# Performance work log

Hardware: AMD Instinct MI355X
Metric: run time of the kernel (lower is better)

Reference implementation:

```python
import jax, jax.numpy as jnp
import numpy as np

NUM_HEADS = 8


def setup_inputs() -> dict:
    key = jax.random.key(0)
    ks = jax.random.split(key, 6)
    B, C, H, W = 64, 512, 16, 16
    x = jax.random.normal(ks[0], (B, C, H, W), dtype=jnp.float32)
    qkv_w = jax.random.normal(ks[1], (3 * C, C), dtype=jnp.float32) * (C ** -0.5)
    qkv_b = jax.random.normal(ks[2], (3 * C,), dtype=jnp.float32) * 0.02
    out_w = jax.random.normal(ks[3], (C, C), dtype=jnp.float32) * (C ** -0.5)
    out_b = jax.random.normal(ks[4], (C,), dtype=jnp.float32) * 0.02
    rel_pos_enc = jax.random.normal(ks[5], (NUM_HEADS, 2 * 16 - 1, 2 * 16 - 1), dtype=jnp.float32) * 0.02
    return {"x": x, "qkv_w": qkv_w, "qkv_b": qkv_b, "out_w": out_w,
            "out_b": out_b, "rel_pos_enc": rel_pos_enc}


def _attention(x, qkv_w, qkv_b, out_w, out_b, rel_pos_enc):
    B, C, H, W = x.shape
    heads = rel_pos_enc.shape[0]
    hd = C // heads
    N = H * W

    # 1x1 conv qkv projection == pointwise GEMM over channels
    qkv = jnp.einsum('bchw,oc->bohw', x, qkv_w) + qkv_b[None, :, None, None]
    q, k, v = jnp.split(qkv, 3, axis=1)  # each (B, C, H, W)
    q = q.reshape(B, heads, hd, N)
    k = k.reshape(B, heads, hd, N)
    v = v.reshape(B, heads, hd, N)

    attn = jnp.einsum('bhdn,bhdm->bhnm', q, k) * (hd ** -0.5)  # (B,h,N,N)

    # gathered 2D relative position bias: bias[head,(h1,w1),(h2,w2)] =
    #   rel_pos_enc[head, h1-h2+15, w1-w2+15]
    h_idx = (jnp.arange(H)[:, None] - jnp.arange(H)[None, :]) + 16 - 1  # (H,H)
    w_idx = (jnp.arange(W)[:, None] - jnp.arange(W)[None, :]) + 16 - 1  # (W,W)
    bias = rel_pos_enc[:, h_idx[:, None, :, None], w_idx[None, :, None, :]]  # (h,H,W,H,W)
    bias = bias.reshape(heads, N, N)

    attn = jax.nn.softmax(attn + bias[None], axis=-1)
    out = jnp.einsum('bhnm,bhdm->bhdn', attn, v).reshape(B, C, H, W)
    out = jnp.einsum('bchw,oc->bohw', out, out_w) + out_b[None, :, None, None]
    return out


def reference(x, qkv_w, qkv_b, out_w, out_b, rel_pos_enc):
    return _attention(x, qkv_w, qkv_b, out_w, out_b, rel_pos_enc)
```

## Files before the change

### kernel.cpp

```cpp
#include <hip/hip_runtime.h>

typedef __attribute__((ext_vector_type(8))) short short8;
typedef __attribute__((ext_vector_type(4))) float floatx4;
typedef __attribute__((ext_vector_type(4))) int   intx4;

#define MFMA16(a,b,c) __builtin_amdgcn_mfma_f32_16x16x32_bf16((a),(b),(c),0,0,0)

static __device__ __forceinline__ unsigned short f2bf(float f){
    unsigned int u = __float_as_uint(f);
    u = (u + 0x7FFFu + ((u >> 16) & 1u)) >> 16;
    return (unsigned short)u;
}

static __device__ __forceinline__ unsigned int pkbf(float lo, float hi){
    unsigned int r;
    asm("v_cvt_pk_bf16_f32 %0, %1, %2" : "=v"(r) : "v"(lo), "v"(hi));
    return r;
}

static __device__ __forceinline__ void async16(const unsigned short* g, const unsigned short* l){
    __builtin_amdgcn_global_load_lds(
        (const __attribute__((address_space(1))) unsigned int*)g,
        (__attribute__((address_space(3))) unsigned int*)l, 16, 0, 0);
}

__global__ __launch_bounds__(256) void k_prep(const float* __restrict__ x,
                                              unsigned short* __restrict__ xT,
                                              const float* __restrict__ qkvw,
                                              unsigned short* __restrict__ wqkv,
                                              const float* __restrict__ outw,
                                              unsigned short* __restrict__ wout){
    __shared__ unsigned short tile[64][78];
    const int bid = blockIdx.x;
    const int tid = threadIdx.x;
    if (bid < 2048){
        const int c0 = (bid & 7) * 64;
        const int n0 = ((bid >> 3) & 3) * 64;
        const int b  = bid >> 5;
        const int chunk = tid & 7;
        const int r     = tid >> 3;
        const float*    src = x  + (size_t)b * 131072;
        unsigned short* dst = xT + (size_t)b * 131072;
#pragma unroll
        for (int it = 0; it < 2; ++it){
            int c = r + it * 32;
            const float* p = src + (size_t)(c0 + c) * 256 + n0 + chunk * 8;
            float4 f0 = *(const float4*)(p);
            float4 f1 = *(const float4*)(p + 4);
            short8 v;
            v[0]=(short)f2bf(f0.x); v[1]=(short)f2bf(f0.y); v[2]=(short)f2bf(f0.z); v[3]=(short)f2bf(f0.w);
            v[4]=(short)f2bf(f1.x); v[5]=(short)f2bf(f1.y); v[6]=(short)f2bf(f1.z); v[7]=(short)f2bf(f1.w);
            *(short8*)&tile[c][chunk * 8] = v;
        }
        __syncthreads();
#pragma unroll
        for (int it = 0; it < 2; ++it){
            int n = r + it * 32;
            short8 o;
#pragma unroll
            for (int e = 0; e < 8; ++e) o[e] = (short)tile[chunk * 8 + e][n];
            *(short8*)(dst + (size_t)(n0 + n) * 512 + c0 + chunk * 8) = o;
        }
    } else {
        int i = (bid - 2048) * 256 + tid;
        const float* s; unsigned short* d; int j;
        if (i < 196608){ s = qkvw; d = wqkv; j = i; }
        else { j = i - 196608; if (j >= 65536) return; s = outw; d = wout; }
        float4 f = *(const float4*)(s + (size_t)j * 4);
        uint2 v;
        v.x = (unsigned int)f2bf(f.x) | ((unsigned int)f2bf(f.y) << 16);
        v.y = (unsigned int)f2bf(f.z) | ((unsigned int)f2bf(f.w) << 16);
        *(uint2*)(d + (size_t)j * 4) = v;
    }
}

__global__ __launch_bounds__(512, 2) void k_fused(const unsigned short* __restrict__ xT,
                                                  const unsigned short* __restrict__ wbf,
                                                  const float* __restrict__ qkvb,
                                                  const float* __restrict__ rel,
                                                  unsigned short* __restrict__ ao){
    __shared__ unsigned short SH[79748];
    const int XS = 0;
    const int WS = 16384;
    const int QS = 28672;
    const int KS = 45056;
    const int VS = 61440;
    float* Relsh = (float*)&SH[77824];

    const int bid  = blockIdx.x;
    const int xcd  = bid & 7;
    const int slot = bid >> 3;
    const int b = xcd * 8 + (slot & 7);
    const int h = slot >> 3;
    const int tid  = threadIdx.x;
    const int wave = tid >> 6;
    const int lane = tid & 63;
    const int lrow = lane & 15;
    const int lgrp = lane >> 4;
    const int mq = wave >> 1;
    const int nh = wave & 1;

    for (int i = tid; i < 961; i += 512) Relsh[i] = rel[h * 961 + i] * 1.44269504f;

    floatx4 acc[4][6];
#pragma unroll
    for (int i = 0; i < 4; ++i)
#pragma unroll
        for (int j = 0; j < 6; ++j){ floatx4 z = {0.f,0.f,0.f,0.f}; acc[i][j] = z; }

    const unsigned short* xb = xT + (size_t)(b * 256) * 512;
    const unsigned short* xsrc[4]; int xdo[4];
#pragma unroll
    for (int c = 0; c < 4; ++c){
        int s   = (c * 8 + wave) * 64 + lane;
        int row = s >> 3, pch = s & 7;
        int sch = pch ^ (row & 7);
        xsrc[c] = xb + (size_t)row * 512 + sch * 8;
        xdo[c]  = (c * 8 + wave) * 512;
    }
    const unsigned short* wsrc[3]; int wdo[3];
#pragma unroll
    for (int c = 0; c < 3; ++c){
        int s   = (c * 8 + wave) * 64 + lane;
        int row = s >> 3, pch = s & 7;
        int sch = pch ^ (row & 7);
        int grow = (row >> 6) * 512 + h * 64 + (row & 63);
        wsrc[c] = wbf + (size_t)grow * 512 + sch * 8;
        wdo[c]  = (c * 8 + wave) * 512;
    }

    auto stageA = [&](int XBs, int WBs, int kk){
#pragma unroll
        for (int c = 0; c < 4; ++c) async16(xsrc[c] + kk, &SH[XBs + xdo[c]]);
#pragma unroll
        for (int c = 0; c < 3; ++c) async16(wsrc[c] + kk, &SH[WBs + wdo[c]]);
    };
    auto compA = [&](int XBs, int WBs){
#pragma unroll
        for (int ks = 0; ks < 2; ++ks){
            short8 af[4], bq[6];
#pragma unroll
            for (int mt = 0; mt < 4; ++mt){
                int row = mq * 64 + mt * 16 + lrow;
                int pch = (ks * 4 + lgrp) ^ (row & 7);
                af[mt] = *(const short8*)&SH[XBs + row * 64 + pch * 8];
            }
#pragma unroll
            for (int nt = 0; nt < 6; ++nt){
                int row = nh * 96 + nt * 16 + lrow;
                int pch = (ks * 4 + lgrp) ^ (row & 7);
                bq[nt] = *(const short8*)&SH[WBs + row * 64 + pch * 8];
            }
#pragma unroll
            for (int mt = 0; mt < 4; ++mt)
#pragma unroll
                for (int nt = 0; nt < 6; ++nt)
                    acc[mt][nt] = MFMA16(af[mt], bq[nt], acc[mt][nt]);
        }
    };

    stageA(XS, WS, 0);
    __syncthreads();
#pragma unroll
    for (int t2 = 0; t2 < 4; ++t2){
        stageA(QS, KS, t2 * 128 + 64);
        compA(XS, WS);
        __syncthreads();
        if (t2 < 3) stageA(XS, WS, t2 * 128 + 128);
        compA(QS, KS);
        __syncthreads();
    }

#pragma unroll
    for (int mt = 0; mt < 4; ++mt){
#pragma unroll
        for (int nt = 0; nt < 6; ++nt){
            int col = nh * 96 + nt * 16 + lrow;
            int seg = col >> 6, off = col & 63;
            float bv = qkvb[seg * 512 + h * 64 + off];
            int token0 = mq * 64 + mt * 16 + lgrp * 4;
            if (seg == 2){
                int lch = token0 >> 3;
                int pch = (lch & 24) | ((lch & 7) ^ (off & 7));
                uint2 vv;
                vv.x = pkbf(acc[mt][nt][0] + bv, acc[mt][nt][1] + bv);
                vv.y = pkbf(acc[mt][nt][2] + bv, acc[mt][nt][3] + bv);
                *(uint2*)&SH[VS + off * 256 + pch * 8 + (lgrp & 1) * 4] = vv;
            } else if (seg == 1){
#pragma unroll
                for (int r = 0; r < 4; ++r){
                    int token = token0 + r;
                    int kslot = (token & ~0x1C) | ((token & 4) << 2) | ((token & 0x18) >> 1);
                    int pch   = (off >> 3) ^ (kslot & 7);
                    SH[KS + kslot * 64 + pch * 8 + (off & 7)] = f2bf(acc[mt][nt][r] + bv);
                }
            } else {
#pragma unroll
                for (int r = 0; r < 4; ++r){
                    int token = token0 + r;
                    int pch   = (off >> 3) ^ (token & 7);
                    SH[QS + token * 64 + pch * 8 + (off & 7)] =
                        f2bf((acc[mt][nt][r] + bv) * 0.18033688f);
                }
            }
        }
    }
    __syncthreads();

    short8 aq[2][2];
#pragma unroll
    for (int pp = 0; pp < 2; ++pp)
#pragma unroll
        for (int kc = 0; kc < 2; ++kc){
            int row = wave * 32 + pp * 16 + lrow;
            int pch = (kc * 4 + lgrp) ^ (row & 7);
            aq[pp][kc] = *(const short8*)&SH[QS + row * 64 + pch * 8];
        }

    unsigned short* aob = ao + (size_t)(b * 256) * 512 + h * 64;
    const int khB = lgrp >> 1;
    const int kwB = (lgrp & 1) * 8;

#pragma unroll
    for (int pp = 0; pp < 2; ++pp){
        floatx4 st[16];
        __builtin_amdgcn_s_setprio(1);
#pragma unroll
        for (int ct = 0; ct < 16; ++ct){
            int row  = ct * 16 + lrow;
            int pch0 = lgrp ^ (row & 7);
            short8 k0 = *(const short8*)&SH[KS + row * 64 + pch0 * 8];
            short8 k1 = *(const short8*)&SH[KS + row * 64 + (pch0 ^ 4) * 8];
            floatx4 z = {0.f,0.f,0.f,0.f};
            z = MFMA16(k0, aq[pp][0], z);
            z = MFMA16(k1, aq[pp][1], z);
            st[ct] = z;
        }
        __builtin_amdgcn_s_setprio(0);

        float sum = 0.f;
        const int rbase = (wave * 2 + pp + 15) * 31 + lrow + 15 - kwB;
#pragma unroll
        for (int ct = 0; ct < 16; ++ct){
            int rb = rbase - (2 * (ct >> 1) + khB) * 31 - 4 * (ct & 1);
#pragma unroll
            for (int r = 0; r < 4; ++r){
                float e = __builtin_amdgcn_exp2f(st[ct][r] + Relsh[rb - r]);
                st[ct][r] = e;
                sum += e;
            }
        }
        sum += __shfl_xor(sum, 16, 64);
        sum += __shfl_xor(sum, 32, 64);
        float inv = 1.f / sum;

        intx4 pf[8];
#pragma unroll
        for (int ms = 0; ms < 8; ++ms){
            intx4 t;
            t.x = (int)pkbf(st[2*ms  ][0], st[2*ms  ][1]);
            t.y = (int)pkbf(st[2*ms  ][2], st[2*ms  ][3]);
            t.z = (int)pkbf(st[2*ms+1][0], st[2*ms+1][1]);
            t.w = (int)pkbf(st[2*ms+1][2], st[2*ms+1][3]);
            pf[ms] = t;
        }

        const int n = wave * 32 + pp * 16 + lrow;
        __builtin_amdgcn_s_setprio(1);
#pragma unroll
        for (int dt = 0; dt < 4; ++dt){
            floatx4 accO = {0.f,0.f,0.f,0.f};
#pragma unroll
            for (int ms = 0; ms < 8; ++ms){
                int row = dt * 16 + lrow;
                int lch = ms * 4 + lgrp;
                int pch = (lch & 24) | ((lch & 7) ^ (row & 7));
                short8 vb = *(const short8*)&SH[VS + row * 256 + pch * 8];
                accO = MFMA16(vb, __builtin_bit_cast(short8, pf[ms]), accO);
            }
            uint2 ov;
            ov.x = pkbf(accO[0] * inv, accO[1] * inv);
            ov.y = pkbf(accO[2] * inv, accO[3] * inv);
            *(uint2*)(aob + (size_t)n * 512 + dt * 16 + lgrp * 4) = ov;
        }
        __builtin_amdgcn_s_setprio(0);
    }
}

__global__ __launch_bounds__(256, 2) void k_out(const unsigned short* __restrict__ ao,
                                                const unsigned short* __restrict__ wbf,
                                                const float* __restrict__ bias,
                                                float* __restrict__ out){
    __shared__ unsigned short Ash[2][2][128][32];
    __shared__ unsigned short Bsh[2][2][128][32];
    const int bid  = blockIdx.x;
    const int xcd  = bid & 7;
    const int slot = bid >> 3;
    const int t0 = (xcd * 16 + (slot & 15)) * 128;
    const int o0 = (slot >> 4) * 128;
    const int tid  = threadIdx.x;
    const int wave = tid >> 6;
    const int lane = tid & 63;
    const int lrow = lane & 15;
    const int wm   = (wave >> 1) * 64;
    const int wn   = (wave & 1) * 64;
    const int ld_row = wave * 32 + (lane >> 2);
    const int ld_col = (((lane & 3) ^ ((lane >> 3) & 3))) * 8;
    const int pcho = (((lane >> 4) ^ ((lrow >> 1) & 3))) * 8;

    floatx4 acc[4][4];
#pragma unroll
    for (int i = 0; i < 4; ++i)
#pragma unroll
        for (int j = 0; j < 4; ++j){ floatx4 z = {0.f,0.f,0.f,0.f}; acc[i][j] = z; }

    const unsigned short* gA = wbf + (size_t)(o0 + ld_row) * 512 + ld_col;
    const unsigned short* gB = ao  + (size_t)(t0 + ld_row) * 512 + ld_col;

    auto stage = [&](int d, int kk){
        async16(gA + kk,                 &Ash[d][0][wave * 32][0]);
        async16(gA + kk + 16 * 512,      &Ash[d][0][wave * 32 + 16][0]);
        async16(gA + kk + 32,            &Ash[d][1][wave * 32][0]);
        async16(gA + kk + 32 + 16 * 512, &Ash[d][1][wave * 32 + 16][0]);
        async16(gB + kk,                 &Bsh[d][0][wave * 32][0]);
        async16(gB + kk + 16 * 512,      &Bsh[d][0][wave * 32 + 16][0]);
        async16(gB + kk + 32,            &Bsh[d][1][wave * 32][0]);
        async16(gB + kk + 32 + 16 * 512, &Bsh[d][1][wave * 32 + 16][0]);
    };
    auto comp = [&](int d){
#pragma unroll
        for (int s = 0; s < 2; ++s){
            short8 af[4], bq[4];
#pragma unroll
            for (int mt = 0; mt < 4; ++mt) af[mt] = *(const short8*)&Ash[d][s][wm + mt*16 + lrow][pcho];
#pragma unroll
            for (int nt = 0; nt < 4; ++nt) bq[nt] = *(const short8*)&Bsh[d][s][wn + nt*16 + lrow][pcho];
#pragma unroll
            for (int mt = 0; mt < 4; ++mt)
#pragma unroll
                for (int nt = 0; nt < 4; ++nt)
                    acc[mt][nt] = MFMA16(af[mt], bq[nt], acc[mt][nt]);
        }
    };

    stage(0, 0);
    __syncthreads();
#pragma unroll
    for (int t2 = 0; t2 < 4; ++t2){
        stage(1, t2 * 128 + 64);
        comp(0);
        __syncthreads();
        if (t2 < 3) stage(0, t2 * 128 + 128);
        comp(1);
        __syncthreads();
    }
#pragma unroll
    for (int mt = 0; mt < 4; ++mt){
        int orow0 = o0 + wm + mt*16 + (lane >> 4) * 4;
#pragma unroll
        for (int nt = 0; nt < 4; ++nt){
            int tcol = t0 + wn + nt*16 + lrow;
            int bb = tcol >> 8, nn = tcol & 255;
#pragma unroll
            for (int r = 0; r < 4; ++r){
                float bv = bias[orow0 + r];
                out[(size_t)(bb * 512 + orow0 + r) * 256 + nn] = acc[mt][nt][r] + bv;
            }
        }
    }
}

extern "C" void kernel_launch(void* const* d_in, const int* in_sizes, int n_in,
                              void* d_out, int out_size, void* d_ws, size_t ws_size,
                              hipStream_t stream){
    const float* x    = (const float*)d_in[0];
    const float* qkvw = (const float*)d_in[1];
    const float* qkvb = (const float*)d_in[2];
    const float* outw = (const float*)d_in[3];
    const float* outb = (const float*)d_in[4];
    const float* rel  = (const float*)d_in[5];
    float* out = (float*)d_out;

    const size_t XT_OFF = 0;
    const size_t AO_OFF = 16777216;
    const size_t W_OFF  = 33554432;
    const size_t NEED   = W_OFF + 4194304;
    if (ws_size < NEED) return;

    char* ws = (char*)d_ws;
    unsigned short* xT = (unsigned short*)(ws + XT_OFF);
    unsigned short* ao = (unsigned short*)(ws + AO_OFF);
    unsigned short* wqkv_bf = (unsigned short*)(ws + W_OFF);
    unsigned short* wout_bf = (unsigned short*)(ws + W_OFF + 2097152);

    hipLaunchKernelGGL(k_prep,  dim3(3072), dim3(256), 0, stream,
                       x, xT, qkvw, wqkv_bf, outw, wout_bf);
    hipLaunchKernelGGL(k_fused, dim3(512),  dim3(512), 0, stream,
                       xT, wqkv_bf, qkvb, rel, ao);
    hipLaunchKernelGGL(k_out,   dim3(512),  dim3(256), 0, stream,
                       ao, wout_bf, outb, out);
}
```

Baseline: 151.2 us.

## Precompute bias matrix as MFMA init and deepen GEMM load pipelining

The prep kernel now expands the relative-position bias into a bf16 (heads,256,256) table, pre-scaled by log2(e). The fused kernel loads this table from global memory and uses it as the MFMA accumulator init, so the per-element shared-memory bias gather and add in the softmax loop go away. Both query sub-tiles are processed together so each V fragment read feeds two MFMAs. The GEMM stage loops in the fused and output kernels now issue two stages ahead and use explicit vmcnt waits with raw barriers instead of __syncthreads. Costs are more global bias traffic, bf16 rounding of the bias, and higher register pressure.

```diff
diff --git a/kernel.cpp b/kernel.cpp
--- a/kernel.cpp
+++ b/kernel.cpp
@@ -29,7 +29,9 @@
                                               const float* __restrict__ qkvw,
                                               unsigned short* __restrict__ wqkv,
                                               const float* __restrict__ outw,
-                                              unsigned short* __restrict__ wout){
+                                              unsigned short* __restrict__ wout,
+                                              const float* __restrict__ rel,
+                                              unsigned short* __restrict__ Bp){
     __shared__ unsigned short tile[64][78];
     const int bid = blockIdx.x;
     const int tid = threadIdx.x;
@@ -61,7 +63,7 @@
             for (int e = 0; e < 8; ++e) o[e] = (short)tile[chunk * 8 + e][n];
             *(short8*)(dst + (size_t)(n0 + n) * 512 + c0 + chunk * 8) = o;
         }
-    } else {
+    } else if (bid < 3072){
         int i = (bid - 2048) * 256 + tid;
         const float* s; unsigned short* d; int j;
         if (i < 196608){ s = qkvw; d = wqkv; j = i; }
@@ -71,21 +73,34 @@
         v.x = (unsigned int)f2bf(f.x) | ((unsigned int)f2bf(f.y) << 16);
         v.y = (unsigned int)f2bf(f.z) | ((unsigned int)f2bf(f.w) << 16);
         *(uint2*)(d + (size_t)j * 4) = v;
+    } else {
+        int idx   = (bid - 3072) * 256 + tid;
+        int h     = idx >> 14;
+        int token = (idx >> 6) & 255;
+        int key0  = (idx & 63) << 2;
+        int th = token >> 4, tw = token & 15;
+        int kh = key0 >> 4,  kw0 = key0 & 15;
+        int base = h * 961 + (th - kh + 15) * 31 + (tw - kw0 + 15);
+        float v0 = rel[base]     * 1.44269504f;
+        float v1 = rel[base - 1] * 1.44269504f;
+        float v2 = rel[base - 2] * 1.44269504f;
+        float v3 = rel[base - 3] * 1.44269504f;
+        uint2 o; o.x = pkbf(v0, v1); o.y = pkbf(v2, v3);
+        *(uint2*)(Bp + (size_t)idx * 4) = o;
     }
 }
 
 __global__ __launch_bounds__(512, 2) void k_fused(const unsigned short* __restrict__ xT,
                                                   const unsigned short* __restrict__ wbf,
                                                   const float* __restrict__ qkvb,
-                                                  const float* __restrict__ rel,
+                                                  const unsigned short* __restrict__ Bp,
                                                   unsigned short* __restrict__ ao){
-    __shared__ unsigned short SH[79748];
+    __shared__ unsigned short SH[77824];
     const int XS = 0;
     const int WS = 16384;
     const int QS = 28672;
     const int KS = 45056;
     const int VS = 61440;
-    float* Relsh = (float*)&SH[77824];
 
     const int bid  = blockIdx.x;
     const int xcd  = bid & 7;
@@ -100,8 +115,6 @@
     const int mq = wave >> 1;
     const int nh = wave & 1;
 
-    for (int i = tid; i < 961; i += 512) Relsh[i] = rel[h * 961 + i] * 1.44269504f;
-
     floatx4 acc[4][6];
 #pragma unroll
     for (int i = 0; i < 4; ++i)
@@ -160,15 +173,27 @@
     };
 
     stageA(XS, WS, 0);
-    __syncthreads();
+    stageA(QS, KS, 64);
 #pragma unroll
     for (int t2 = 0; t2 < 4; ++t2){
-        stageA(QS, KS, t2 * 128 + 64);
+        asm volatile("s_waitcnt vmcnt(7)" ::: "memory");
+        __builtin_amdgcn_s_barrier();
+        asm volatile("" ::: "memory");
         compA(XS, WS);
-        __syncthreads();
-        if (t2 < 3) stageA(XS, WS, t2 * 128 + 128);
+        asm volatile("" ::: "memory");
+        if (t2 < 3){
+            __builtin_amdgcn_s_barrier();
+            stageA(XS, WS, t2 * 128 + 128);
+            asm volatile("s_waitcnt vmcnt(7)" ::: "memory");
+        } else {
+            asm volatile("s_waitcnt vmcnt(0)" ::: "memory");
+        }
+        __builtin_amdgcn_s_barrier();
+        asm volatile("" ::: "memory");
         compA(QS, KS);
-        __syncthreads();
+        asm volatile("" ::: "memory");
+        __builtin_amdgcn_s_barrier();
+        if (t2 < 3) stageA(QS, KS, t2 * 128 + 192);
     }
 
 #pragma unroll
@@ -217,74 +242,106 @@
             aq[pp][kc] = *(const short8*)&SH[QS + row * 64 + pch * 8];
         }
 
+    const unsigned short* bp0 = Bp + ((size_t)h * 256 + wave * 32 + lrow) * 256;
+
+    floatx4 st0[16], st1[16];
+    __builtin_amdgcn_s_setprio(1);
+#pragma unroll
+    for (int ct = 0; ct < 16; ++ct){
+        int key0 = 32 * (ct >> 1) + 8 * lgrp + 4 * (ct & 1);
+        uint2 bA = *(const uint2*)(bp0 + key0);
+        uint2 bB = *(const uint2*)(bp0 + 4096 + key0);
+        int row  = ct * 16 + lrow;
+        int pch0 = lgrp ^ (row & 7);
+        short8 k0 = *(const short8*)&SH[KS + row * 64 + pch0 * 8];
+        short8 k1 = *(const short8*)&SH[KS + row * 64 + (pch0 ^ 4) * 8];
+        floatx4 z0, z1;
+        z0[0] = __uint_as_float(bA.x << 16);
+        z0[1] = __uint_as_float(bA.x & 0xFFFF0000u);
+        z0[2] = __uint_as_float(bA.y << 16);
+        z0[3] = __uint_as_float(bA.y & 0xFFFF0000u);
+        z1[0] = __uint_as_float(bB.x << 16);
+        z1[1] = __uint_as_float(bB.x & 0xFFFF0000u);
+        z1[2] = __uint_as_float(bB.y << 16);
+        z1[3] = __uint_as_float(bB.y & 0xFFFF0000u);
+        z0 = MFMA16(k0, aq[0][0], z0);
+        z0 = MFMA16(k1, aq[0][1], z0);
+        z1 = MFMA16(k0, aq[1][0], z1);
+        z1 = MFMA16(k1, aq[1][1], z1);
+        st0[ct] = z0; st1[ct] = z1;
+    }
+    __builtin_amdgcn_s_setprio(0);
+
+    float inv0, inv1;
+    {
+        float p0=0.f,p1=0.f,p2=0.f,p3=0.f;
+#pragma unroll
+        for (int ct = 0; ct < 16; ++ct){
+            float e0 = __builtin_amdgcn_exp2f(st0[ct][0]); st0[ct][0]=e0; p0+=e0;
+            float e1 = __builtin_amdgcn_exp2f(st0[ct][1]); st0[ct][1]=e1; p1+=e1;
+            float e2 = __builtin_amdgcn_exp2f(st0[ct][2]); st0[ct][2]=e2; p2+=e2;
+            float e3 = __builtin_amdgcn_exp2f(st0[ct][3]); st0[ct][3]=e3; p3+=e3;
+        }
+        float s = (p0+p1)+(p2+p3);
+        s += __shfl_xor(s, 16, 64);
+        s += __shfl_xor(s, 32, 64);
+        inv0 = 1.f / s;
+    }
+    {
+        float p0=0.f,p1=0.f,p2=0.f,p3=0.f;
+#pragma unroll
+        for (int ct = 0; ct < 16; ++ct){
+            float e0 = __builtin_amdgcn_exp2f(st1[ct][0]); st1[ct][0]=e0; p0+=e0;
+            float e1 = __builtin_amdgcn_exp2f(st1[ct][1]); st1[ct][1]=e1; p1+=e1;
+            float e2 = __builtin_amdgcn_exp2f(st1[ct][2]); st1[ct][2]=e2; p2+=e2;
+            float e3 = __builtin_amdgcn_exp2f(st1[ct][3]); st1[ct][3]=e3; p3+=e3;
+        }
+        float s = (p0+p1)+(p2+p3);
+        s += __shfl_xor(s, 16, 64);
+        s += __shfl_xor(s, 32, 64);
+        inv1 = 1.f / s;
+    }
+
+    intx4 pf0[8], pf1[8];
+#pragma unroll
+    for (int ms = 0; ms < 8; ++ms){
+        intx4 t0_, t1_;
+        t0_.x = (int)pkbf(st0[2*ms  ][0], st0[2*ms  ][1]);
+        t0_.y = (int)pkbf(st0[2*ms  ][2], st0[2*ms  ][3]);
+        t0_.z = (int)pkbf(st0[2*ms+1][0], st0[2*ms+1][1]);
+        t0_.w = (int)pkbf(st0[2*ms+1][2], st0[2*ms+1][3]);
+        pf0[ms] = t0_;
+        t1_.x = (int)pkbf(st1[2*ms  ][0], st1[2*ms  ][1]);
+        t1_.y = (int)pkbf(st1[2*ms  ][2], st1[2*ms  ][3]);
+        t1_.z = (int)pkbf(st1[2*ms+1][0], st1[2*ms+1][1]);
+        t1_.w = (int)pkbf(st1[2*ms+1][2], st1[2*ms+1][3]);
+        pf1[ms] = t1_;
+    }
+
     unsigned short* aob = ao + (size_t)(b * 256) * 512 + h * 64;
-    const int khB = lgrp >> 1;
-    const int kwB = (lgrp & 1) * 8;
-
-#pragma unroll
-    for (int pp = 0; pp < 2; ++pp){
-        floatx4 st[16];
-        __builtin_amdgcn_s_setprio(1);
-#pragma unroll
-        for (int ct = 0; ct < 16; ++ct){
-            int row  = ct * 16 + lrow;
-            int pch0 = lgrp ^ (row & 7);
-            short8 k0 = *(const short8*)&SH[KS + row * 64 + pch0 * 8];
-            short8 k1 = *(const short8*)&SH[KS + row * 64 + (pch0 ^ 4) * 8];
-            floatx4 z = {0.f,0.f,0.f,0.f};
-            z = MFMA16(k0, aq[pp][0], z);
-            z = MFMA16(k1, aq[pp][1], z);
-            st[ct] = z;
-        }
-        __builtin_amdgcn_s_setprio(0);
-
-        float sum = 0.f;
-        const int rbase = (wave * 2 + pp + 15) * 31 + lrow + 15 - kwB;
-#pragma unroll
-        for (int ct = 0; ct < 16; ++ct){
-            int rb = rbase - (2 * (ct >> 1) + khB) * 31 - 4 * (ct & 1);
-#pragma unroll
-            for (int r = 0; r < 4; ++r){
-                float e = __builtin_amdgcn_exp2f(st[ct][r] + Relsh[rb - r]);
-                st[ct][r] = e;
-                sum += e;
-            }
-        }
-        sum += __shfl_xor(sum, 16, 64);
-        sum += __shfl_xor(sum, 32, 64);
-        float inv = 1.f / sum;
-
-        intx4 pf[8];
+    const int n0 = wave * 32 + lrow;
+    __builtin_amdgcn_s_setprio(1);
+#pragma unroll
+    for (int dt = 0; dt < 4; ++dt){
+        floatx4 a0 = {0.f,0.f,0.f,0.f}, a1 = {0.f,0.f,0.f,0.f};
 #pragma unroll
         for (int ms = 0; ms < 8; ++ms){
-            intx4 t;
-            t.x = (int)pkbf(st[2*ms  ][0], st[2*ms  ][1]);
-            t.y = (int)pkbf(st[2*ms  ][2], st[2*ms  ][3]);
-            t.z = (int)pkbf(st[2*ms+1][0], st[2*ms+1][1]);
-            t.w = (int)pkbf(st[2*ms+1][2], st[2*ms+1][3]);
-            pf[ms] = t;
-        }
-
-        const int n = wave * 32 + pp * 16 + lrow;
-        __builtin_amdgcn_s_setprio(1);
-#pragma unroll
-        for (int dt = 0; dt < 4; ++dt){
-            floatx4 accO = {0.f,0.f,0.f,0.f};
-#pragma unroll
-            for (int ms = 0; ms < 8; ++ms){
-                int row = dt * 16 + lrow;
-                int lch = ms * 4 + lgrp;
-                int pch = (lch & 24) | ((lch & 7) ^ (row & 7));
-                short8 vb = *(const short8*)&SH[VS + row * 256 + pch * 8];
-                accO = MFMA16(vb, __builtin_bit_cast(short8, pf[ms]), accO);
-            }
-            uint2 ov;
-            ov.x = pkbf(accO[0] * inv, accO[1] * inv);
-            ov.y = pkbf(accO[2] * inv, accO[3] * inv);
-            *(uint2*)(aob + (size_t)n * 512 + dt * 16 + lgrp * 4) = ov;
-        }
-        __builtin_amdgcn_s_setprio(0);
-    }
+            int row = dt * 16 + lrow;
+            int lch = ms * 4 + lgrp;
+            int pch = (lch & 24) | ((lch & 7) ^ (row & 7));
+            short8 vb = *(const short8*)&SH[VS + row * 256 + pch * 8];
+            a0 = MFMA16(vb, __builtin_bit_cast(short8, pf0[ms]), a0);
+            a1 = MFMA16(vb, __builtin_bit_cast(short8, pf1[ms]), a1);
+        }
+        uint2 o0, o1;
+        o0.x = pkbf(a0[0] * inv0, a0[1] * inv0);
+        o0.y = pkbf(a0[2] * inv0, a0[3] * inv0);
+        *(uint2*)(aob + (size_t)n0 * 512 + dt * 16 + lgrp * 4) = o0;
+        o1.x = pkbf(a1[0] * inv1, a1[1] * inv1);
+        o1.y = pkbf(a1[2] * inv1, a1[3] * inv1);
+        *(uint2*)(aob + (size_t)(n0 + 16) * 512 + dt * 16 + lgrp * 4) = o1;
+    }
+    __builtin_amdgcn_s_setprio(0);
 }
 
 __global__ __launch_bounds__(256, 2) void k_out(const unsigned short* __restrict__ ao,
@@ -344,15 +401,27 @@
     };
 
     stage(0, 0);
-    __syncthreads();
+    stage(1, 64);
 #pragma unroll
     for (int t2 = 0; t2 < 4; ++t2){
-        stage(1, t2 * 128 + 64);
+        asm volatile("s_waitcnt vmcnt(8)" ::: "memory");
+        __builtin_amdgcn_s_barrier();
+        asm volatile("" ::: "memory");
         comp(0);
-        __syncthreads();
-        if (t2 < 3) stage(0, t2 * 128 + 128);
+        asm volatile("" ::: "memory");
+        if (t2 < 3){
+            __builtin_amdgcn_s_barrier();
+            stage(0, t2 * 128 + 128);
+            asm volatile("s_waitcnt vmcnt(8)" ::: "memory");
+        } else {
+            asm volatile("s_waitcnt vmcnt(0)" ::: "memory");
+        }
+        __builtin_amdgcn_s_barrier();
+        asm volatile("" ::: "memory");
         comp(1);
-        __syncthreads();
+        asm volatile("" ::: "memory");
+        __builtin_amdgcn_s_barrier();
+        if (t2 < 3) stage(1, t2 * 128 + 192);
     }
 #pragma unroll
     for (int mt = 0; mt < 4; ++mt){
@@ -392,11 +461,12 @@
     unsigned short* ao = (unsigned short*)(ws + AO_OFF);
     unsigned short* wqkv_bf = (unsigned short*)(ws + W_OFF);
     unsigned short* wout_bf = (unsigned short*)(ws + W_OFF + 2097152);
-
-    hipLaunchKernelGGL(k_prep,  dim3(3072), dim3(256), 0, stream,
-                       x, xT, qkvw, wqkv_bf, outw, wout_bf);
+    unsigned short* Bp      = (unsigned short*)(ws + W_OFF + 2621440);
+
+    hipLaunchKernelGGL(k_prep,  dim3(3584), dim3(256), 0, stream,
+                       x, xT, qkvw, wqkv_bf, outw, wout_bf, rel, Bp);
     hipLaunchKernelGGL(k_fused, dim3(512),  dim3(512), 0, stream,
-                       xT, wqkv_bf, qkvb, rel, ao);
+                       xT, wqkv_bf, qkvb, Bp, ao);
     hipLaunchKernelGGL(k_out,   dim3(512),  dim3(256), 0, stream,
                        ao, wout_bf, outb, out);
 }
```

Result: no change. 151.6 us (+0.2%).
